# Optimization experiments

Hardware: AMD Instinct MI355X
Metric: run time of the kernel (lower is better)

## Reference

```python
import jax, jax.numpy as jnp
import numpy as np

ORDER = 2


def _get_moments(image, order):
    # image: (B, C, H, W)
    B, C, H, W = image.shape
    # per-item mean and unbiased variance over (C,H,W) (torch .mean()/.var() defaults)
    mean = image.mean(axis=(1, 2, 3))                      # (B,)
    var = image.var(axis=(1, 2, 3), ddof=1)                # (B,) unbiased, as torch
    std = jnp.sqrt(var)                                    # (B,)
    # Faithful to source bug: inner loops read image[m, i, j] where image = image_ori[m],
    # i.e. channel index == batch index -> diagonal slice image_ori[m, m, :, :]
    idx = jnp.arange(B)
    x = image[idx, idx]                                    # (B, H, W)
    z = (x - mean[:, None, None]) / std[:, None, None]     # standardized pixels
    denom = float(C * H * W) ** order                      # (C*H*W)**order normalizer
    moment = (z ** order).sum(axis=(1, 2)) / denom         # (B,)
    return moment.sum()                                    # scalar, summed over batch


def setup_inputs() -> dict:
    key = jax.random.key(0)
    k1, k2 = jax.random.split(key)
    shape = (8, 8, 1024, 1024)
    image1 = jax.random.normal(k1, shape, dtype=jnp.float32)
    image2 = jax.random.normal(k2, shape, dtype=jnp.float32)
    return {"image1": image1, "image2": image2}


def reference(image1, image2):
    m1 = _get_moments(image1, ORDER)
    m2 = _get_moments(image2, ORDER)
    # nn.L1Loss on scalars -> absolute difference
    return jnp.abs(m1 - m2)
```

## Files before the change

### kernel.cpp

```cpp
#include <hip/hip_runtime.h>

constexpr int B = 8, C = 8;
constexpr long long PLANE = 1024LL * 1024LL;
constexpr long long NCHW  = (long long)C * PLANE;
constexpr int BLOCKS_PER_PLANE = 16;
constexpr int THREADS = 256;
constexpr int F4_PER_BLOCK = (int)(PLANE / BLOCKS_PER_PLANE / 4);
constexpr int ITERS = F4_PER_BLOCK / THREADS;

__global__ __launch_bounds__(THREADS) void moments_pass1(
    const float* __restrict__ img0, const float* __restrict__ img1,
    double* __restrict__ acc) {
  int gb    = blockIdx.x;
  int plane = gb / BLOCKS_PER_PLANE;
  int chunk = gb % BLOCKS_PER_PLANE;
  int imgi  = plane >> 6;
  int rem   = plane & 63;
  int b     = rem >> 3;
  int c     = rem & 7;

  const float* base = (imgi ? img1 : img0)
                    + (long long)rem * PLANE
                    + (long long)chunk * (PLANE / BLOCKS_PER_PLANE);
  const float4* p = (const float4*)base;

  double s1 = 0.0, s2 = 0.0;
  int tid = threadIdx.x;
#pragma unroll 8
  for (int it = 0; it < ITERS; ++it) {
    float4 v = p[it * THREADS + tid];
    double a = (double)v.x, bb = (double)v.y, cc = (double)v.z, d = (double)v.w;
    s1 += (a + bb) + (cc + d);
    s2 = fma(a, a, s2); s2 = fma(bb, bb, s2);
    s2 = fma(cc, cc, s2); s2 = fma(d, d, s2);
  }

  for (int off = 32; off > 0; off >>= 1) {
    s1 += __shfl_down(s1, off, 64);
    s2 += __shfl_down(s2, off, 64);
  }

  __shared__ double sh1[4], sh2[4];
  int wave = tid >> 6, lane = tid & 63;
  if (lane == 0) { sh1[wave] = s1; sh2[wave] = s2; }
  __syncthreads();
  if (tid == 0) {
    double t1 = (sh1[0] + sh1[1]) + (sh1[2] + sh1[3]);
    double t2 = (sh2[0] + sh2[1]) + (sh2[2] + sh2[3]);
    double* a4 = acc + ((imgi * B + b) * 4);
    atomicAdd(&a4[0], t1);
    atomicAdd(&a4[1], t2);
    if (c == b) {
      atomicAdd(&a4[2], t1);
      atomicAdd(&a4[3], t2);
    }
  }
}

__global__ void moments_pass2(const double* __restrict__ acc,
                              float* __restrict__ out) {
  if (blockIdx.x == 0 && threadIdx.x == 0) {
    const double N    = (double)NCHW;
    const double Npix = (double)PLANE;
    const double denom = N * N;
    double res[2];
    for (int i = 0; i < 2; ++i) {
      double msum = 0.0;
      for (int m = 0; m < B; ++m) {
        const double* a = acc + (i * B + m) * 4;
        double S1 = a[0], S2 = a[1], D1 = a[2], D2 = a[3];
        double mean = S1 / N;
        double var  = (S2 - S1 * S1 / N) / (N - 1.0);
        double ssq  = D2 - 2.0 * mean * D1 + Npix * mean * mean;
        msum += ssq / var / denom;
      }
      res[i] = msum;
    }
    out[0] = (float)fabs(res[0] - res[1]);
  }
}

extern "C" void kernel_launch(void* const* d_in, const int* in_sizes, int n_in,
                              void* d_out, int out_size, void* d_ws, size_t ws_size,
                              hipStream_t stream) {
  const float* img0 = (const float*)d_in[0];
  const float* img1 = (const float*)d_in[1];
  double* acc = (double*)d_ws;
  hipMemsetAsync(d_ws, 0, 2 * B * 4 * sizeof(double), stream);
  moments_pass1<<<2 * B * C * BLOCKS_PER_PLANE, THREADS, 0, stream>>>(img0, img1, acc);
  moments_pass2<<<1, 64, 0, stream>>>(acc, (float*)d_out);
}
```

Measured before the change: 503.5 us.

## Replace atomics and memset with per-block partials and parallel final reduction

Each block now writes its partial sums to its own slot instead of doing double atomics into a zeroed accumulator. This removes the memset launch and atomic contention, and pass2 becomes a 1024-thread reduction over the 2048 partials. The main loop also uses nontemporal vector loads and splits the accumulators into independent chains to shorten the FMA dependency. The kernel is bound by reading 512 MB of memory, so the gain is likely small.

Result: faster. 467.6 us (-7.1%).

```diff
diff --git a/kernel.cpp b/kernel.cpp
--- a/kernel.cpp
+++ b/kernel.cpp
@@ -4,36 +4,43 @@
 constexpr long long PLANE = 1024LL * 1024LL;
 constexpr long long NCHW  = (long long)C * PLANE;
 constexpr int BLOCKS_PER_PLANE = 16;
+constexpr int NBLOCKS = 2 * B * C * BLOCKS_PER_PLANE;
 constexpr int THREADS = 256;
 constexpr int F4_PER_BLOCK = (int)(PLANE / BLOCKS_PER_PLANE / 4);
 constexpr int ITERS = F4_PER_BLOCK / THREADS;
 
+typedef float f32x4 __attribute__((ext_vector_type(4)));
+
 __global__ __launch_bounds__(THREADS) void moments_pass1(
     const float* __restrict__ img0, const float* __restrict__ img1,
-    double* __restrict__ acc) {
+    double2* __restrict__ part) {
   int gb    = blockIdx.x;
   int plane = gb / BLOCKS_PER_PLANE;
   int chunk = gb % BLOCKS_PER_PLANE;
   int imgi  = plane >> 6;
   int rem   = plane & 63;
-  int b     = rem >> 3;
-  int c     = rem & 7;
 
   const float* base = (imgi ? img1 : img0)
                     + (long long)rem * PLANE
                     + (long long)chunk * (PLANE / BLOCKS_PER_PLANE);
-  const float4* p = (const float4*)base;
+  const f32x4* p = (const f32x4*)base;
 
-  double s1 = 0.0, s2 = 0.0;
   int tid = threadIdx.x;
+  double s1a = 0.0, s1b = 0.0;
+  double q0 = 0.0, q1 = 0.0, q2 = 0.0, q3 = 0.0;
 #pragma unroll 8
   for (int it = 0; it < ITERS; ++it) {
-    float4 v = p[it * THREADS + tid];
-    double a = (double)v.x, bb = (double)v.y, cc = (double)v.z, d = (double)v.w;
-    s1 += (a + bb) + (cc + d);
-    s2 = fma(a, a, s2); s2 = fma(bb, bb, s2);
-    s2 = fma(cc, cc, s2); s2 = fma(d, d, s2);
+    f32x4 v = __builtin_nontemporal_load(p + it * THREADS + tid);
+    double a = (double)v.x, b2 = (double)v.y, c2 = (double)v.z, d = (double)v.w;
+    s1a += a + b2;
+    s1b += c2 + d;
+    q0 = fma(a, a, q0);
+    q1 = fma(b2, b2, q1);
+    q2 = fma(c2, c2, q2);
+    q3 = fma(d, d, q3);
   }
+  double s1 = s1a + s1b;
+  double s2 = (q0 + q1) + (q2 + q3);
 
   for (int off = 32; off > 0; off >>= 1) {
     s1 += __shfl_down(s1, off, 64);
@@ -47,36 +54,50 @@
   if (tid == 0) {
     double t1 = (sh1[0] + sh1[1]) + (sh1[2] + sh1[3]);
     double t2 = (sh2[0] + sh2[1]) + (sh2[2] + sh2[3]);
-    double* a4 = acc + ((imgi * B + b) * 4);
-    atomicAdd(&a4[0], t1);
-    atomicAdd(&a4[1], t2);
-    if (c == b) {
-      atomicAdd(&a4[2], t1);
-      atomicAdd(&a4[3], t2);
-    }
+    part[gb] = make_double2(t1, t2);
   }
 }
 
-__global__ void moments_pass2(const double* __restrict__ acc,
-                              float* __restrict__ out) {
-  if (blockIdx.x == 0 && threadIdx.x == 0) {
+__global__ __launch_bounds__(1024) void moments_pass2(
+    const double2* __restrict__ part, float* __restrict__ out) {
+  int tid  = threadIdx.x;
+  int w    = tid >> 6;
+  int lane = tid & 63;
+  int b    = w & 7;
+
+  const double2 p0 = part[w * 128 + lane];
+  const double2 p1 = part[w * 128 + 64 + lane];
+  int c0 = lane >> 4;
+  int c1 = c0 + 4;
+
+  double s1 = p0.x + p1.x;
+  double s2 = p0.y + p1.y;
+  double d1 = (c0 == b ? p0.x : 0.0) + (c1 == b ? p1.x : 0.0);
+  double d2 = (c0 == b ? p0.y : 0.0) + (c1 == b ? p1.y : 0.0);
+
+  for (int off = 32; off > 0; off >>= 1) {
+    s1 += __shfl_down(s1, off, 64);
+    s2 += __shfl_down(s2, off, 64);
+    d1 += __shfl_down(d1, off, 64);
+    d2 += __shfl_down(d2, off, 64);
+  }
+
+  __shared__ double msh[16];
+  if (lane == 0) {
     const double N    = (double)NCHW;
     const double Npix = (double)PLANE;
     const double denom = N * N;
-    double res[2];
-    for (int i = 0; i < 2; ++i) {
-      double msum = 0.0;
-      for (int m = 0; m < B; ++m) {
-        const double* a = acc + (i * B + m) * 4;
-        double S1 = a[0], S2 = a[1], D1 = a[2], D2 = a[3];
-        double mean = S1 / N;
-        double var  = (S2 - S1 * S1 / N) / (N - 1.0);
-        double ssq  = D2 - 2.0 * mean * D1 + Npix * mean * mean;
-        msum += ssq / var / denom;
-      }
-      res[i] = msum;
-    }
-    out[0] = (float)fabs(res[0] - res[1]);
+    double mean = s1 / N;
+    double var  = (s2 - s1 * s1 / N) / (N - 1.0);
+    double ssq  = d2 - 2.0 * mean * d1 + Npix * mean * mean;
+    msh[w] = ssq / var / denom;
+  }
+  __syncthreads();
+  if (tid == 0) {
+    double m0 = 0.0, m1 = 0.0;
+    for (int i = 0; i < 8; ++i)  m0 += msh[i];
+    for (int i = 8; i < 16; ++i) m1 += msh[i];
+    out[0] = (float)fabs(m0 - m1);
   }
 }
 
@@ -85,8 +106,7 @@
                               hipStream_t stream) {
   const float* img0 = (const float*)d_in[0];
   const float* img1 = (const float*)d_in[1];
-  double* acc = (double*)d_ws;
-  hipMemsetAsync(d_ws, 0, 2 * B * 4 * sizeof(double), stream);
-  moments_pass1<<<2 * B * C * BLOCKS_PER_PLANE, THREADS, 0, stream>>>(img0, img1, acc);
-  moments_pass2<<<1, 64, 0, stream>>>(acc, (float*)d_out);
+  double2* part = (double2*)d_ws;
+  moments_pass1<<<NBLOCKS, THREADS, 0, stream>>>(img0, img1, part);
+  moments_pass2<<<1, 1024, 0, stream>>>(part, (float*)d_out);
 }
```
